# Optimization experiments

Hardware: AMD Instinct MI355X
Metric: run time of the kernel (lower is better)

Reference implementation:

```python
import jax, jax.numpy as jnp
import numpy as np
from jax import lax

RATE = 2
KSIZE = 3
SCALE = 10.0
RATES = (1, 2, 4, 8)
EPS_NORM = 1e-4
EPS_CLAMP = 1e-8


def extract_patches(x, k, s, pad):
    # x: [B, C, H, W] -> patches [B, L, C, k, k], L in row-major (H', W') order
    x = jnp.pad(x, ((0, 0), (0, 0), (pad, pad), (pad, pad)))
    B, C, H, W = x.shape
    ii = jnp.arange(0, H - k + 1, s)[:, None] + jnp.arange(k)[None, :]  # [Ho, k]
    jj = jnp.arange(0, W - k + 1, s)[:, None] + jnp.arange(k)[None, :]  # [Wo, k]
    p = x[:, :, ii, :]            # [B, C, Ho, k, W]
    p = p[:, :, :, :, jj]         # [B, C, Ho, k, Wo, k]
    p = p.transpose(0, 2, 4, 1, 3, 5)  # [B, Ho, Wo, C, k, k]
    return p.reshape(B, -1, C, k, k)


def _forward(x1, x2, mask, fws, fbs):
    B, C1, H1, W1 = x1.shape
    _, C2, H2, W2 = x2.shape
    kernel = 2 * RATE  # 4

    raw_w = extract_patches(x1, kernel, RATE, 1)   # [B, L, C1, 4, 4]
    w = extract_patches(x2, KSIZE, 1, 1)           # [B, L, C2, 3, 3]
    # mask already at (H2, W2): bilinear align_corners resize to same size is identity
    m = extract_patches(mask, KSIZE, 1, 1)         # [B, L, 1, 3, 3]
    mm = (jnp.mean(m, axis=(2, 3, 4)) == 0.0).astype(x2.dtype)  # [B, L]; 1 = fully valid patch

    def per_sample(xi, wi, rwi, mi):
        # xi: [C2,H2,W2]; wi: [L,C2,3,3]; rwi: [L,C1,4,4]; mi: [L]
        norm = jnp.sqrt(jnp.sum(wi * wi, axis=(1, 2, 3), keepdims=True))
        wn = wi / jnp.maximum(norm, EPS_NORM)
        # correlation: L normalized patches act as conv filters over xi
        yi = lax.conv_general_dilated(
            xi[None], wn, (1, 1), ((1, 1), (1, 1)),
            dimension_numbers=('NCHW', 'OIHW', 'NCHW'))[0]   # [L, H2, W2]
        mi3 = mi[:, None, None]
        yi = jax.nn.softmax(yi * mi3 * SCALE, axis=0) * mi3   # softmax over patch dim L
        yi = jnp.clip(yi, EPS_CLAMP)
        # conv_transpose2d(yi, rwi, stride=rate, padding=1) via lhs-dilated conv
        wt = jnp.flip(rwi, axis=(-2, -1)).transpose(1, 0, 2, 3)  # [C1, L, 4, 4]
        pad = kernel - 1 - 1  # k - 1 - padding = 2
        out = lax.conv_general_dilated(
            yi[None], wt, (1, 1), ((pad, pad), (pad, pad)),
            lhs_dilation=(RATE, RATE),
            dimension_numbers=('NCHW', 'OIHW', 'NCHW'))[0] / 4.0  # [C1, H1, W1]
        return out

    y = jax.vmap(per_sample)(x2, w, raw_w, mm)  # [B, C1, H1, W1]

    outs = []
    for fw, fb, r in zip(fws, fbs, RATES):
        o = lax.conv_general_dilated(
            y, fw, (1, 1), ((r, r), (r, r)), rhs_dilation=(r, r),
            dimension_numbers=('NCHW', 'OIHW', 'NCHW'))
        outs.append(jax.nn.relu(o + fb[None, :, None, None]))
    return jnp.concatenate(outs, axis=1)  # [B, 64, H1, W1]


def setup_inputs() -> dict:
    key = jax.random.key(0)
    ks = jax.random.split(key, 12)
    B, C, H1, H2 = 2, 128, 128, 64
    inp = {
        'x1': jax.random.normal(ks[0], (B, C, H1, H1), jnp.float32),
        'x2': jax.random.normal(ks[1], (B, C, H2, H2), jnp.float32),
        'mask': jax.random.randint(ks[2], (B, 1, H2, H2), 0, 2).astype(jnp.float32),
    }
    for i in range(4):
        inp[f'fw{i}'] = jax.random.normal(ks[3 + i], (16, 128, 3, 3), jnp.float32) * 0.05
        inp[f'fb{i}'] = jnp.zeros((16,), jnp.float32)
    return inp


def reference(x1, x2, mask, fw0, fb0, fw1, fb1, fw2, fb2, fw3, fb3):
    return _forward(x1, x2, mask, (fw0, fw1, fw2, fw3), (fb0, fb1, fb2, fb3))
```

## Files before the change

### kernel.cpp

```cpp
#include <hip/hip_runtime.h>
#include <cstdint>

#define BATCH 2
#define CCH 128
#define H2 64
#define NP 4096
#define H1 128
#define YPB (CCH*H1*H1)

typedef __attribute__((ext_vector_type(8))) short bf16x8;
typedef __attribute__((ext_vector_type(4))) float f32x4;

__global__ void __launch_bounds__(1024) k1_compact(const float* __restrict__ mask,
                                                   int* __restrict__ cnt,
                                                   int* __restrict__ idx)
{
    __shared__ int widx[16][256];
    __shared__ int wcnt[16];
    __shared__ int woff[16];
    int b    = blockIdx.x;
    int t    = threadIdx.x;
    int lane = t & 63;
    int w    = t >> 6;
    const float* mb = mask + b * (H2*H2);
    int count = 0;
    #pragma unroll
    for (int it = 0; it < 4; ++it) {
        int p = w*256 + it*64 + lane;
        int ph = p >> 6, pw = p & 63;
        float s = 0.f;
        #pragma unroll
        for (int dh = -1; dh <= 1; ++dh) {
            int r = ph + dh;
            if ((unsigned)r < (unsigned)H2) {
                #pragma unroll
                for (int dw = -1; dw <= 1; ++dw) {
                    int c = pw + dw;
                    if ((unsigned)c < (unsigned)H2) s += mb[r*H2 + c];
                }
            }
        }
        bool flag = (s == 0.0f);
        unsigned long long m = __ballot(flag);
        int pre = __popcll(m & ((1ull << lane) - 1ull));
        if (flag) widx[w][count + pre] = p;
        count += __popcll(m);
    }
    if (lane == 0) wcnt[w] = count;
    __syncthreads();
    if (t == 0) {
        int acc = 0;
        #pragma unroll
        for (int i = 0; i < 16; ++i) { woff[i] = acc; acc += wcnt[i]; }
        cnt[b] = acc;
    }
    __syncthreads();
    int base = b*NP + woff[w];
    int n = wcnt[w];
    for (int i = lane; i < n; i += 64)
        idx[base + i] = widx[w][i];
}

__global__ void k2_norms(const float* __restrict__ x2, const int* __restrict__ cnt,
                         const int* __restrict__ idx, float* __restrict__ rnorm)
{
    int cnt0 = cnt[0], cnt1 = cnt[1];
    int total = cnt0 + cnt1;
    int lane = threadIdx.x;
    for (int item = blockIdx.x; item < total; item += gridDim.x) {
        int b, j;
        if (item < cnt0) { b = 0; j = item; } else { b = 1; j = item - cnt0; }
        int p = idx[b*NP + j];
        int qh = p >> 6, qw = p & 63;
        const float* xb = x2 + (size_t)b * CCH * H2 * H2;
        float s = 0.f;
        for (int c = lane; c < CCH; c += 64) {
            const float* xc = xb + (size_t)c * H2 * H2;
            #pragma unroll
            for (int dh = -1; dh <= 1; ++dh) {
                int r = qh + dh;
                if ((unsigned)r < (unsigned)H2) {
                    #pragma unroll
                    for (int dw = -1; dw <= 1; ++dw) {
                        int cc = qw + dw;
                        if ((unsigned)cc < (unsigned)H2) { float v = xc[r*H2 + cc]; s += v*v; }
                    }
                }
            }
        }
        #pragma unroll
        for (int off = 32; off > 0; off >>= 1) s += __shfl_down(s, off, 64);
        if (lane == 0) rnorm[b*NP + j] = 1.0f / fmaxf(sqrtf(s), 1e-4f);
    }
}

__global__ void __launch_bounds__(256) k3_scores(const float* __restrict__ x2,
    const int* __restrict__ cnt, const int* __restrict__ idx,
    const float* __restrict__ rnorm, float* __restrict__ S, int base, int CQ)
{
    __shared__ float f[9*CCH];
    __shared__ float psum[4][64];
    int tid  = threadIdx.x;
    int lane = tid & 63;
    int wv   = tid >> 6;
    int cnt0 = cnt[0], cnt1 = cnt[1];
    int nb0 = min(max(cnt0 - base, 0), CQ);
    int nb1 = min(max(cnt1 - base, 0), CQ);
    long units = (long)(nb0 + nb1) * 64;
    for (long u = blockIdx.x; u < units; u += gridDim.x) {
        int item = (int)(u >> 6);
        int h    = (int)(u & 63);
        int b, jq;
        if (item < nb0) { b = 0; jq = item; } else { b = 1; jq = item - nb0; }
        int jg = base + jq;
        int p = idx[b*NP + jg];
        int qh = p >> 6, qw = p & 63;
        float rn = rnorm[b*NP + jg];
        const float* xb = x2 + (size_t)b * CCH * H2 * H2;
        for (int t2 = tid; t2 < 9*CCH; t2 += 256) {
            int k = t2 >> 7, c = t2 & 127;
            int dh = k / 3, dw = k % 3;
            int r = qh + dh - 1, cc = qw + dw - 1;
            float v = 0.f;
            if ((unsigned)r < (unsigned)H2 && (unsigned)cc < (unsigned)H2)
                v = xb[((size_t)c*H2 + r)*H2 + cc];
            f[t2] = v * rn;
        }
        __syncthreads();
        int c0 = wv * 32;
        float a0=0.f,a1=0.f,a2=0.f,a3=0.f,a4=0.f,a5=0.f,a6=0.f,a7=0.f;
        #pragma unroll
        for (int k = 0; k < 9; ++k) {
            int dh = k/3, dw = k%3;
            int rr = h + dh - 1;
            int cc = lane + dw - 1;
            if ((unsigned)rr < (unsigned)H2 && (unsigned)cc < (unsigned)H2) {
                const float* xp = xb + (size_t)c0*H2*H2 + (size_t)rr*H2 + cc;
                const float* fp = f + k*CCH + c0;
                #pragma unroll
                for (int c = 0; c < 32; c += 8) {
                    a0 += xp[(size_t)(c+0)*H2*H2] * fp[c+0];
                    a1 += xp[(size_t)(c+1)*H2*H2] * fp[c+1];
                    a2 += xp[(size_t)(c+2)*H2*H2] * fp[c+2];
                    a3 += xp[(size_t)(c+3)*H2*H2] * fp[c+3];
                    a4 += xp[(size_t)(c+4)*H2*H2] * fp[c+4];
                    a5 += xp[(size_t)(c+5)*H2*H2] * fp[c+5];
                    a6 += xp[(size_t)(c+6)*H2*H2] * fp[c+6];
                    a7 += xp[(size_t)(c+7)*H2*H2] * fp[c+7];
                }
            }
        }
        psum[wv][lane] = ((a0+a1)+(a2+a3)) + ((a4+a5)+(a6+a7));
        __syncthreads();
        if (wv == 0) {
            float sv = (psum[0][lane] + psum[1][lane])
                     + (psum[2][lane] + psum[3][lane]);
            S[((size_t)(b*CQ + jq))*NP + h*64 + lane] = sv;
        }
        __syncthreads();
    }
}

__global__ void k3b_stats(const float* __restrict__ S, const int* __restrict__ cnt,
                          float* __restrict__ M, float* __restrict__ D,
                          int base, int CQ, int init)
{
    int t = blockIdx.x*blockDim.x + threadIdx.x;
    if (t >= BATCH*NP) return;
    int b = t >> 12, s = t & (NP-1);
    int n = min(max(cnt[b] - base, 0), CQ);
    float m, d;
    if (init) { m = 0.f; d = (float)(NP - cnt[b]); }
    else {
        if (n == 0) return;
        m = M[t]; d = D[t];
    }
    for (int j = 0; j < n; ++j) {
        float l = 10.f * S[((size_t)(b*CQ + j))*NP + s];
        if (l > m) { d = d*__expf(m - l) + 1.f; m = l; }
        else       { d += __expf(l - m); }
    }
    M[t] = m; D[t] = d;
}

#define TJ 32
__global__ void __launch_bounds__(128) k5_paste(const float* __restrict__ A,
    const int* __restrict__ cnt, const int* __restrict__ idx,
    const float* __restrict__ x1,
    const float* __restrict__ M, const float* __restrict__ D,
    float* __restrict__ y, int base, int CQ, int accumulate)
{
    __shared__ float sA[TJ][2][64];
    __shared__ int   sQ[TJ];
    int ow = threadIdx.x;
    int ck = blockIdx.x;
    int oh = blockIdx.y;
    int b  = blockIdx.z;
    int n = min(max(cnt[b] - base, 0), CQ);

    if (n == 0) {
        if (!accumulate) {
            size_t obase = ((size_t)(b*CCH + ck*16)*H1 + oh)*H1 + ow;
            #pragma unroll
            for (int co = 0; co < 16; ++co) y[obase + (size_t)co*H1*H1] = 0.f;
        }
        return;
    }

    int ohp = oh & 1;
    int ih0 = (oh + 1) >> 1;
    int ihv0 = (ih0 <= 63);
    int ihv1 = (ih0 >= 1);
    int iw0 = (ow + 1) >> 1;
    int iwv0 = (iw0 <= 63);
    int iwv1 = (iw0 >= 1);

    float acc[16];
    #pragma unroll
    for (int o = 0; o < 16; ++o) acc[o] = 0.f;

    const float* x1c = x1 + ((size_t)(b*CCH + ck*16))*H1*H1;
    const float* Mb = M + b*NP;
    const float* Db = D + b*NP;

    for (int j0 = 0; j0 < n; j0 += TJ) {
        int m = min(TJ, n - j0);
        if (ow < m) sQ[ow] = idx[b*NP + base + j0 + ow];
        for (int u = ow; u < m*128; u += 128) {
            int j  = u >> 7;
            int s  = (u >> 6) & 1;
            int iw = u & 63;
            int ih = ih0 - s;
            int ihc = min(max(ih, 0), 63);
            float v = 0.f;
            if (s == 0 ? ihv0 : ihv1) {
                int scol = ihc*64 + iw;
                float sv = A[((size_t)(b*CQ + j0 + j))*NP + scol];
                v = __expf(10.f*sv - Mb[scol]) / Db[scol];
            }
            sA[j][s][iw] = v;
        }
        __syncthreads();
        for (int j = 0; j < m; ++j) {
            int qp = sQ[j];
            int qh = qp >> 6, qw = qp & 63;
            int rr0 = 2*qh - ohp;
            int rr1 = rr0 + 2;
            int cc0 = 2*qw - (ow & 1);
            int cc1 = cc0 + 2;
            int rv0 = ihv0 && ((unsigned)rr0 < (unsigned)H1);
            int rv1 = ihv1 && ((unsigned)rr1 < (unsigned)H1);
            int cv0 = iwv0 && ((unsigned)cc0 < (unsigned)H1);
            int cv1 = iwv1 && ((unsigned)cc1 < (unsigned)H1);
            int iwc0 = min(max(iw0, 0), 63);
            int iwc1 = min(max(iw0 - 1, 0), 63);
            float w00 = (rv0 && cv0) ? sA[j][0][iwc0] : 0.f;
            float w01 = (rv0 && cv1) ? sA[j][0][iwc1] : 0.f;
            float w10 = (rv1 && cv0) ? sA[j][1][iwc0] : 0.f;
            float w11 = (rv1 && cv1) ? sA[j][1][iwc1] : 0.f;
            int r0c = min(max(rr0, 0), H1-1) * H1;
            int r1c = min(max(rr1, 0), H1-1) * H1;
            int c0c = min(max(cc0, 0), H1-1);
            int c1c = min(max(cc1, 0), H1-1);
            int off00 = r0c + c0c;
            int off01 = r0c + c1c;
            int off10 = r1c + c0c;
            int off11 = r1c + c1c;
            #pragma unroll
            for (int co = 0; co < 16; ++co) {
                const float* pc = x1c + (size_t)co*H1*H1;
                acc[co] += w00*pc[off00] + w01*pc[off01]
                         + w10*pc[off10] + w11*pc[off11];
            }
        }
        __syncthreads();
    }
    size_t obase = ((size_t)(b*CCH + ck*16)*H1 + oh)*H1 + ow;
    #pragma unroll
    for (int co = 0; co < 16; ++co) {
        size_t oi = obase + (size_t)co*H1*H1;
        float v = 0.25f*acc[co];
        y[oi] = accumulate ? (y[oi] + v) : v;
    }
}

__global__ void __launch_bounds__(128) k_ybt(const float* __restrict__ y,
                                             uint16_t* __restrict__ ybt)
{
    __shared__ uint16_t tile[128*130 + 2];
    int row = blockIdx.x & 127;
    int b   = blockIdx.x >> 7;
    int col = threadIdx.x;
    const float* yb = y + (size_t)b*YPB + (size_t)row*H1;
    for (int c = 0; c < CCH; ++c) {
        float v = yb[(size_t)c*H1*H1 + col];
        uint32_t u = __float_as_uint(v);
        u = (u + 0x7FFFu + ((u >> 16) & 1u)) >> 16;
        tile[col*130 + c] = (uint16_t)u;
    }
    __syncthreads();
    uint32_t* dst = (uint32_t*)(ybt + ((size_t)(b*H1 + row))*H1*CCH);
    const uint32_t* tl = (const uint32_t*)tile;
    for (int i = threadIdx.x; i < H1*CCH/2; i += 128) {
        int cidx = i >> 6;
        int chh  = i & 63;
        dst[i] = tl[cidx*65 + chh];
    }
}

__global__ void k_wprep(const float* __restrict__ fw0, const float* __restrict__ fw1,
                        const float* __restrict__ fw2, const float* __restrict__ fw3,
                        uint16_t* __restrict__ wbf)
{
    int kstep = blockIdx.x % 36;
    int g     = blockIdx.x / 36;
    const float* fw = (g==0)?fw0:(g==1)?fw1:(g==2)?fw2:fw3;
    int l  = threadIdx.x;
    int co = l & 15;
    int kg = l >> 4;
    int tap = kstep >> 2;
    int c0  = (kstep & 3) * 32;
    uint16_t* dst = wbf + ((size_t)(g*36 + kstep)*64 + l)*8;
    #pragma unroll
    for (int i = 0; i < 8; ++i) {
        int ch = c0 + kg*8 + i;
        float v = fw[((size_t)co*CCH + ch)*9 + tap];
        uint32_t u = __float_as_uint(v);
        u = (u + 0x7FFFu + ((u >> 16) & 1u)) >> 16;
        dst[i] = (uint16_t)u;
    }
}

__global__ void __launch_bounds__(256) k6_mfma(const uint16_t* __restrict__ ybt,
    const uint16_t* __restrict__ wbf,
    const float* __restrict__ fb0, const float* __restrict__ fb1,
    const float* __restrict__ fb2, const float* __restrict__ fb3,
    float* __restrict__ out)
{
    int t    = threadIdx.x;
    int lane = t & 63;
    int wv   = t >> 6;
    int L    = blockIdx.x;
    int xcd  = L & 7;
    int slot = L >> 3;
    int b    = xcd >> 2;
    int band = xcd & 3;
    int g    = slot >> 5;
    int oh   = band*32 + (slot & 31);
    int r    = 1 << g;
    const float* fb = (g==0)?fb0:(g==1)?fb1:(g==2)?fb2:fb3;
    int n15 = lane & 15;
    int kg  = lane >> 4;
    int ow0 = wv * 32;
    f32x4 acc0 = {0.f,0.f,0.f,0.f};
    f32x4 acc1 = {0.f,0.f,0.f,0.f};
    const uint16_t* wbase = wbf + (size_t)g*36*512 + lane*8;
    const uint16_t* ybase = ybt + (size_t)b*H1*H1*CCH;
    const bf16x8 zero = {0,0,0,0,0,0,0,0};
    for (int ks = 0; ks < 36; ++ks) {
        int tap = ks >> 2;
        int c0  = (ks & 3) * 32;
        int rr  = oh + r*(tap/3 - 1);
        bool rok = (unsigned)rr < (unsigned)H1;
        int rrc = min(max(rr, 0), H1-1);
        bf16x8 af = *(const bf16x8*)(wbase + (size_t)ks*512);
        int chb = c0 + kg*8;
        const uint16_t* yrow = ybase + (size_t)rrc*H1*CCH;
        int cc0 = ow0 + n15 + r*(tap%3 - 1);
        int cc1 = cc0 + 16;
        bool v0 = rok && (unsigned)cc0 < (unsigned)H1;
        bool v1 = rok && (unsigned)cc1 < (unsigned)H1;
        int cc0c = min(max(cc0, 0), H1-1);
        int cc1c = min(max(cc1, 0), H1-1);
        bf16x8 bf0 = *(const bf16x8*)(yrow + (size_t)cc0c*CCH + chb);
        bf16x8 bf1 = *(const bf16x8*)(yrow + (size_t)cc1c*CCH + chb);
        if (!v0) bf0 = zero;
        if (!v1) bf1 = zero;
        acc0 = __builtin_amdgcn_mfma_f32_16x16x32_bf16(af, bf0, acc0, 0, 0, 0);
        acc1 = __builtin_amdgcn_mfma_f32_16x16x32_bf16(af, bf1, acc1, 0, 0, 0);
    }
    #pragma unroll
    for (int j = 0; j < 4; ++j) {
        int co = kg*4 + j;
        float bias = fb[co];
        size_t o0 = ((size_t)(b*64 + g*16 + co)*H1 + oh)*H1 + ow0 + n15;
        out[o0]      = fmaxf(acc0[j] + bias, 0.f);
        out[o0 + 16] = fmaxf(acc1[j] + bias, 0.f);
    }
}

extern "C" void kernel_launch(void* const* d_in, const int* in_sizes, int n_in,
                              void* d_out, int out_size, void* d_ws, size_t ws_size,
                              hipStream_t stream)
{
    const float* x1   = (const float*)d_in[0];
    const float* x2   = (const float*)d_in[1];
    const float* mask = (const float*)d_in[2];
    const float* fw0 = (const float*)d_in[3];
    const float* fb0 = (const float*)d_in[4];
    const float* fw1 = (const float*)d_in[5];
    const float* fb1 = (const float*)d_in[6];
    const float* fw2 = (const float*)d_in[7];
    const float* fb2 = (const float*)d_in[8];
    const float* fw3 = (const float*)d_in[9];
    const float* fb3 = (const float*)d_in[10];
    float* out = (float*)d_out;
    char* ws = (char*)d_ws;

    size_t off = 0;
    auto alloc = [&](size_t bytes) { size_t o = off; off += (bytes + 255) & ~(size_t)255; return o; };
    size_t cnt_off = alloc(BATCH*sizeof(int));
    size_t idx_off = alloc((size_t)BATCH*NP*sizeof(int));
    size_t rn_off  = alloc((size_t)BATCH*NP*sizeof(float));
    size_t M_off   = alloc((size_t)BATCH*NP*sizeof(float));
    size_t D_off   = alloc((size_t)BATCH*NP*sizeof(float));
    size_t y_off   = alloc((size_t)BATCH*YPB*sizeof(float));
    size_t ybt_off = alloc((size_t)BATCH*H1*H1*CCH*sizeof(uint16_t));
    size_t wbf_off = alloc((size_t)4*36*512*sizeof(uint16_t));
    size_t remain = (ws_size > off) ? (ws_size - off) : 0;
    int CQ = (int)(remain / ((size_t)BATCH*NP*sizeof(float)));
    if (CQ > NP) CQ = NP;
    if (CQ < 1) CQ = 1;
    size_t S_off = off;
    int NCH = (NP + CQ - 1) / CQ;

    int* cnt   = (int*)(ws + cnt_off);
    int* idx   = (int*)(ws + idx_off);
    float* rnm = (float*)(ws + rn_off);
    float* Mv  = (float*)(ws + M_off);
    float* Dv  = (float*)(ws + D_off);
    float* y   = (float*)(ws + y_off);
    uint16_t* ybt = (uint16_t*)(ws + ybt_off);
    uint16_t* wbf = (uint16_t*)(ws + wbf_off);
    float* S   = (float*)(ws + S_off);

    k1_compact<<<BATCH, 1024, 0, stream>>>(mask, cnt, idx);
    k2_norms<<<256, 64, 0, stream>>>(x2, cnt, idx, rnm);
    k_wprep<<<4*36, 64, 0, stream>>>(fw0, fw1, fw2, fw3, wbf);
    for (int ch = NCH - 1; ch >= 0; --ch) {
        k3_scores<<<2048, 256, 0, stream>>>(x2, cnt, idx, rnm, S, ch*CQ, CQ);
        k3b_stats<<<(BATCH*NP+255)/256, 256, 0, stream>>>(S, cnt, Mv, Dv, ch*CQ, CQ,
                                                          ch == NCH - 1 ? 1 : 0);
    }
    for (int ch = 0; ch < NCH; ++ch) {
        if (ch > 0)
            k3_scores<<<2048, 256, 0, stream>>>(x2, cnt, idx, rnm, S, ch*CQ, CQ);
        k5_paste<<<dim3(8, H1, BATCH), 128, 0, stream>>>(S, cnt, idx, x1, Mv, Dv, y,
                                                         ch*CQ, CQ, ch > 0 ? 1 : 0);
    }
    k_ybt<<<BATCH*H1, 128, 0, stream>>>(y, ybt);
    k6_mfma<<<1024, 256, 0, stream>>>(ybt, wbf, fb0, fb1, fb2, fb3, out);
}
```

Before: 129.1 us.

## Fuse bf16 transpose into paste kernel and compute two rows per MFMA block

```diff
diff --git a/kernel.cpp b/kernel.cpp
--- a/kernel.cpp
+++ b/kernel.cpp
@@ -10,6 +10,12 @@
 
 typedef __attribute__((ext_vector_type(8))) short bf16x8;
 typedef __attribute__((ext_vector_type(4))) float f32x4;
+
+__device__ __forceinline__ uint16_t f2bf(float v) {
+    uint32_t u = __float_as_uint(v);
+    u = (u + 0x7FFFu + ((u >> 16) & 1u)) >> 16;
+    return (uint16_t)u;
+}
 
 __global__ void __launch_bounds__(1024) k1_compact(const float* __restrict__ mask,
                                                    int* __restrict__ cnt,
@@ -188,7 +194,8 @@
     const int* __restrict__ cnt, const int* __restrict__ idx,
     const float* __restrict__ x1,
     const float* __restrict__ M, const float* __restrict__ D,
-    float* __restrict__ y, int base, int CQ, int accumulate)
+    float* __restrict__ y, uint16_t* __restrict__ ybt,
+    int base, int CQ, int accumulate)
 {
     __shared__ float sA[TJ][2][64];
     __shared__ int   sQ[TJ];
@@ -198,11 +205,16 @@
     int b  = blockIdx.z;
     int n = min(max(cnt[b] - base, 0), CQ);
 
+    size_t obase = ((size_t)(b*CCH + ck*16)*H1 + oh)*H1 + ow;
+    uint16_t* yt = ybt + (((size_t)(b*H1 + oh))*H1 + ow)*CCH + ck*16;
+
     if (n == 0) {
         if (!accumulate) {
-            size_t obase = ((size_t)(b*CCH + ck*16)*H1 + oh)*H1 + ow;
             #pragma unroll
-            for (int co = 0; co < 16; ++co) y[obase + (size_t)co*H1*H1] = 0.f;
+            for (int co = 0; co < 16; ++co) {
+                y[obase + (size_t)co*H1*H1] = 0.f;
+                yt[co] = 0;
+            }
         }
         return;
     }
@@ -275,36 +287,13 @@
         }
         __syncthreads();
     }
-    size_t obase = ((size_t)(b*CCH + ck*16)*H1 + oh)*H1 + ow;
     #pragma unroll
     for (int co = 0; co < 16; ++co) {
         size_t oi = obase + (size_t)co*H1*H1;
         float v = 0.25f*acc[co];
-        y[oi] = accumulate ? (y[oi] + v) : v;
-    }
-}
-
-__global__ void __launch_bounds__(128) k_ybt(const float* __restrict__ y,
-                                             uint16_t* __restrict__ ybt)
-{
-    __shared__ uint16_t tile[128*130 + 2];
-    int row = blockIdx.x & 127;
-    int b   = blockIdx.x >> 7;
-    int col = threadIdx.x;
-    const float* yb = y + (size_t)b*YPB + (size_t)row*H1;
-    for (int c = 0; c < CCH; ++c) {
-        float v = yb[(size_t)c*H1*H1 + col];
-        uint32_t u = __float_as_uint(v);
-        u = (u + 0x7FFFu + ((u >> 16) & 1u)) >> 16;
-        tile[col*130 + c] = (uint16_t)u;
-    }
-    __syncthreads();
-    uint32_t* dst = (uint32_t*)(ybt + ((size_t)(b*H1 + row))*H1*CCH);
-    const uint32_t* tl = (const uint32_t*)tile;
-    for (int i = threadIdx.x; i < H1*CCH/2; i += 128) {
-        int cidx = i >> 6;
-        int chh  = i & 63;
-        dst[i] = tl[cidx*65 + chh];
+        float fin = accumulate ? (y[oi] + v) : v;
+        y[oi] = fin;
+        yt[co] = f2bf(fin);
     }
 }
 
@@ -324,10 +313,7 @@
     #pragma unroll
     for (int i = 0; i < 8; ++i) {
         int ch = c0 + kg*8 + i;
-        float v = fw[((size_t)co*CCH + ch)*9 + tap];
-        uint32_t u = __float_as_uint(v);
-        u = (u + 0x7FFFu + ((u >> 16) & 1u)) >> 16;
-        dst[i] = (uint16_t)u;
+        dst[i] = f2bf(fw[((size_t)co*CCH + ch)*9 + tap]);
     }
 }
 
@@ -345,47 +331,65 @@
     int slot = L >> 3;
     int b    = xcd >> 2;
     int band = xcd & 3;
-    int g    = slot >> 5;
-    int oh   = band*32 + (slot & 31);
+    int g    = slot >> 4;
+    int pr   = slot & 15;
+    int oh0  = band*32 + pr*2;
+    int oh1  = oh0 + 1;
     int r    = 1 << g;
     const float* fb = (g==0)?fb0:(g==1)?fb1:(g==2)?fb2:fb3;
     int n15 = lane & 15;
     int kg  = lane >> 4;
     int ow0 = wv * 32;
-    f32x4 acc0 = {0.f,0.f,0.f,0.f};
-    f32x4 acc1 = {0.f,0.f,0.f,0.f};
+    f32x4 a00 = {0.f,0.f,0.f,0.f};
+    f32x4 a01 = {0.f,0.f,0.f,0.f};
+    f32x4 a10 = {0.f,0.f,0.f,0.f};
+    f32x4 a11 = {0.f,0.f,0.f,0.f};
     const uint16_t* wbase = wbf + (size_t)g*36*512 + lane*8;
     const uint16_t* ybase = ybt + (size_t)b*H1*H1*CCH;
     const bf16x8 zero = {0,0,0,0,0,0,0,0};
     for (int ks = 0; ks < 36; ++ks) {
         int tap = ks >> 2;
         int c0  = (ks & 3) * 32;
-        int rr  = oh + r*(tap/3 - 1);
-        bool rok = (unsigned)rr < (unsigned)H1;
-        int rrc = min(max(rr, 0), H1-1);
+        int dr  = r*(tap/3 - 1);
+        int rr0 = oh0 + dr;
+        int rr1 = oh1 + dr;
+        bool rok0 = (unsigned)rr0 < (unsigned)H1;
+        bool rok1 = (unsigned)rr1 < (unsigned)H1;
+        int rr0c = min(max(rr0, 0), H1-1);
+        int rr1c = min(max(rr1, 0), H1-1);
         bf16x8 af = *(const bf16x8*)(wbase + (size_t)ks*512);
         int chb = c0 + kg*8;
-        const uint16_t* yrow = ybase + (size_t)rrc*H1*CCH;
+        const uint16_t* yrow0 = ybase + (size_t)rr0c*H1*CCH;
+        const uint16_t* yrow1 = ybase + (size_t)rr1c*H1*CCH;
         int cc0 = ow0 + n15 + r*(tap%3 - 1);
         int cc1 = cc0 + 16;
-        bool v0 = rok && (unsigned)cc0 < (unsigned)H1;
-        bool v1 = rok && (unsigned)cc1 < (unsigned)H1;
+        bool c0ok = (unsigned)cc0 < (unsigned)H1;
+        bool c1ok = (unsigned)cc1 < (unsigned)H1;
         int cc0c = min(max(cc0, 0), H1-1);
         int cc1c = min(max(cc1, 0), H1-1);
-        bf16x8 bf0 = *(const bf16x8*)(yrow + (size_t)cc0c*CCH + chb);
-        bf16x8 bf1 = *(const bf16x8*)(yrow + (size_t)cc1c*CCH + chb);
-        if (!v0) bf0 = zero;
-        if (!v1) bf1 = zero;
-        acc0 = __builtin_amdgcn_mfma_f32_16x16x32_bf16(af, bf0, acc0, 0, 0, 0);
-        acc1 = __builtin_amdgcn_mfma_f32_16x16x32_bf16(af, bf1, acc1, 0, 0, 0);
+        bf16x8 b00 = *(const bf16x8*)(yrow0 + (size_t)cc0c*CCH + chb);
+        bf16x8 b01 = *(const bf16x8*)(yrow0 + (size_t)cc1c*CCH + chb);
+        bf16x8 b10 = *(const bf16x8*)(yrow1 + (size_t)cc0c*CCH + chb);
+        bf16x8 b11 = *(const bf16x8*)(yrow1 + (size_t)cc1c*CCH + chb);
+        if (!(rok0 && c0ok)) b00 = zero;
+        if (!(rok0 && c1ok)) b01 = zero;
+        if (!(rok1 && c0ok)) b10 = zero;
+        if (!(rok1 && c1ok)) b11 = zero;
+        a00 = __builtin_amdgcn_mfma_f32_16x16x32_bf16(af, b00, a00, 0, 0, 0);
+        a01 = __builtin_amdgcn_mfma_f32_16x16x32_bf16(af, b01, a01, 0, 0, 0);
+        a10 = __builtin_amdgcn_mfma_f32_16x16x32_bf16(af, b10, a10, 0, 0, 0);
+        a11 = __builtin_amdgcn_mfma_f32_16x16x32_bf16(af, b11, a11, 0, 0, 0);
     }
     #pragma unroll
     for (int j = 0; j < 4; ++j) {
         int co = kg*4 + j;
         float bias = fb[co];
-        size_t o0 = ((size_t)(b*64 + g*16 + co)*H1 + oh)*H1 + ow0 + n15;
-        out[o0]      = fmaxf(acc0[j] + bias, 0.f);
-        out[o0 + 16] = fmaxf(acc1[j] + bias, 0.f);
+        size_t r0 = ((size_t)(b*64 + g*16 + co)*H1 + oh0)*H1 + ow0 + n15;
+        size_t r1 = ((size_t)(b*64 + g*16 + co)*H1 + oh1)*H1 + ow0 + n15;
+        out[r0]      = fmaxf(a00[j] + bias, 0.f);
+        out[r0 + 16] = fmaxf(a01[j] + bias, 0.f);
+        out[r1]      = fmaxf(a10[j] + bias, 0.f);
+        out[r1 + 16] = fmaxf(a11[j] + bias, 0.f);
     }
 }
 
@@ -446,8 +450,7 @@
         if (ch > 0)
             k3_scores<<<2048, 256, 0, stream>>>(x2, cnt, idx, rnm, S, ch*CQ, CQ);
         k5_paste<<<dim3(8, H1, BATCH), 128, 0, stream>>>(S, cnt, idx, x1, Mv, Dv, y,
-                                                         ch*CQ, CQ, ch > 0 ? 1 : 0);
-    }
-    k_ybt<<<BATCH*H1, 128, 0, stream>>>(y, ybt);
-    k6_mfma<<<1024, 256, 0, stream>>>(ybt, wbf, fb0, fb1, fb2, fb3, out);
-}
+                                                         ybt, ch*CQ, CQ, ch > 0 ? 1 : 0);
+    }
+    k6_mfma<<<512, 256, 0, stream>>>(ybt, wbf, fb0, fb1, fb2, fb3, out);
+}
```

Measured after the change: 132.7 us. 1.03x slower.
